# Performance work log

Measured on AMD Instinct MI355X. Metric: run time of the kernel, lower is better.

## Reference

```python
import jax, jax.numpy as jnp
from jax import lax
import numpy as np

DN = ('NCHW', 'OIHW', 'NCHW')
K = 3          # deformable kernel size
DG = 4         # deform groups
EXP = 4        # InvBottle expansion


def conv_offset(x, w1, w2, b2):
    """InvBottle with diff=True: depthwise-expanded 3x3 conv, diff correction, 1x1 conv."""
    B, C, H, W = x.shape
    _x = lax.conv_general_dilated(x, w1, (1, 1), ((1, 1), (1, 1)),
                                  dimension_numbers=DN, feature_group_count=C)  # [B,4C,H,W]
    # diff_conv: subtract grouped 1x1 conv with the kernel-summed weight
    wsum = w1.sum((2, 3)).reshape(1, EXP * C, 1, 1)          # [1,4C,1,1]
    xd = _x - jnp.repeat(x, EXP, axis=1) * wsum              # group g uses input channel g
    t = lax.conv_general_dilated(xd, w2, (1, 1), ((0, 0), (0, 0)), dimension_numbers=DN)
    return t + b2.reshape(1, -1, 1, 1)                       # [B,72,H,W]


def deform_depthwise(x, off, w, pad=1):
    """Depthwise DeformConv2d (groups=C, deform_groups=DG), stride=1, dilation=1."""
    B, C, H, W = x.shape
    Cg = C // DG
    off = off.reshape(B, DG, K * K, 2, H, W)                 # (dy, dx) interleaved per tap
    dy, dx = off[:, :, :, 0], off[:, :, :, 1]                # [B,DG,9,H,W]
    ky = (jnp.arange(K * K) // K).reshape(1, 1, K * K, 1, 1).astype(x.dtype)
    kx = (jnp.arange(K * K) % K).reshape(1, 1, K * K, 1, 1).astype(x.dtype)
    py = jnp.arange(H, dtype=x.dtype).reshape(1, 1, 1, H, 1) - pad + ky + dy
    px = jnp.arange(W, dtype=x.dtype).reshape(1, 1, 1, 1, W) - pad + kx + dx

    y0 = jnp.floor(py)
    x0 = jnp.floor(px)
    wy = py - y0
    wx = px - x0

    xg = x.reshape(B, DG, Cg, H * W)

    def gather(yy, xx):
        valid = ((yy >= 0) & (yy < H) & (xx >= 0) & (xx < W)).astype(x.dtype)
        yc = jnp.clip(yy, 0, H - 1).astype(jnp.int32)
        xc = jnp.clip(xx, 0, W - 1).astype(jnp.int32)
        idx = (yc * W + xc).reshape(B, DG, 1, K * K * H * W)
        v = jnp.take_along_axis(xg, jnp.broadcast_to(idx, (B, DG, Cg, K * K * H * W)), axis=3)
        return v.reshape(B, DG, Cg, K * K, H, W) * valid[:, :, None]

    val = (gather(y0, x0) * ((1 - wy) * (1 - wx))[:, :, None]
           + gather(y0, x0 + 1) * ((1 - wy) * wx)[:, :, None]
           + gather(y0 + 1, x0) * (wy * (1 - wx))[:, :, None]
           + gather(y0 + 1, x0 + 1) * (wy * wx)[:, :, None])   # [B,DG,Cg,9,H,W]

    val = val.reshape(B, C, K * K, H, W)
    return jnp.einsum('bckhw,ck->bchw', val, w.reshape(C, K * K))


def setup_inputs() -> dict:
    key = jax.random.key(0)
    ks = jax.random.split(key, 6)
    B, C, H, W = 2, 64, 192, 192
    x1 = jax.random.normal(ks[0], (B, C, H, W), jnp.float32)
    w_off1 = jax.random.normal(ks[1], (EXP * C, 1, K, K), jnp.float32) * 0.1
    w_off2 = jax.random.normal(ks[2], (DG * 2 * K * K, EXP * C, 1, 1), jnp.float32) * 0.1
    b_off2 = jax.random.normal(ks[3], (DG * 2 * K * K,), jnp.float32) * 0.1
    w_def = jax.random.normal(ks[4], (C, 1, K, K), jnp.float32) * 0.1
    w_out = jax.random.normal(ks[5], (C, C, 1, 1), jnp.float32) * 0.1
    return {'x1': x1, 'w_off1': w_off1, 'w_off2': w_off2, 'b_off2': b_off2,
            'w_def': w_def, 'w_out': w_out}


def reference(x1, w_off1, w_off2, b_off2, w_def, w_out):
    x2 = x1
    C = x1.shape[1]
    t = conv_offset(x1, w_off1, w_off2, b_off2)              # [B,72,H,W]
    y = deform_depthwise(x1, t, w_def)                       # DeformConv2d, groups=C
    # diff_conv against the deform conv's kernel-summed depthwise weight
    y = y - x2 * w_def.sum((1, 2, 3)).reshape(1, C, 1, 1)
    m = jnp.einsum('bchw,oc->bohw', y, w_out.reshape(w_out.shape[0], C))  # 1x1, no bias
    return (x1, m)
```

## Files before the change

### kernel.cpp

```cpp
#include <hip/hip_runtime.h>

#define BN   2
#define CN   64
#define HN   192
#define WN   192
#define HWN  36864
#define OCN  256
#define JCN  72
#define SN   32

#define DROWS 8
#define XH    17
#define XW    42
#define XRT   4
#define XCL   4

#define PGRPS 2304

typedef __attribute__((ext_vector_type(8))) short bf16x8;
typedef __attribute__((ext_vector_type(8))) unsigned short u16x8;
typedef __attribute__((ext_vector_type(4))) float f32x4;

__device__ __forceinline__ unsigned short f2bf(float f) {
    union { float f; unsigned u; } v; v.f = f;
    unsigned r = v.u + 0x7fffu + ((v.u >> 16) & 1u);
    return (unsigned short)(r >> 16);
}

__global__ __launch_bounds__(256) void k_prep(const float* __restrict__ w2,
                                              const float* __restrict__ w_out,
                                              const float* __restrict__ w1,
                                              unsigned short* __restrict__ w2mf,
                                              unsigned short* __restrict__ w_outmf,
                                              float* __restrict__ w1p) {
    int idx = blockIdx.x * 256 + threadIdx.x;
    if (idx < 20480) {
        int j  = idx & 7;
        int l  = (idx >> 3) & 63;
        int ts = idx >> 9;
        int tm = ts >> 3, s = ts & 7;
        int jrow = tm * 16 + (l & 15);
        int k    = s * 32 + (l >> 4) * 8 + j;
        float v = (jrow < JCN) ? w2[jrow * OCN + k] : 0.f;
        w2mf[idx] = f2bf(v);
    } else if (idx < 24576) {
        int r  = idx - 20480;
        int j  = r & 7;
        int l  = (r >> 3) & 63;
        int ts = r >> 9;
        int tm = ts >> 1, s = ts & 1;
        int m  = tm * 16 + (l & 15);
        int k  = s * 32 + (l >> 4) * 8 + j;
        w_outmf[r] = f2bf(w_out[m * CN + k]);
    } else if (idx < 26624) {
        int r = idx - 24576;
        int o = r >> 3, kk = r & 7;
        int k = kk < 4 ? kk : kk + 1;
        w1p[r] = w1[o * 9 + k];
    }
}

__global__ __launch_bounds__(256, 4) void k_offsets(const float* __restrict__ x,
                                                    const float* __restrict__ w1p,
                                                    const unsigned short* __restrict__ w2mf,
                                                    const float* __restrict__ b2,
                                                    float* __restrict__ t_out,
                                                    float* __restrict__ x_copy) {
    const int f  = blockIdx.x + 3 * blockIdx.y + 576 * blockIdx.z;
    const int nn = (f & 7) * 144 + (f >> 3);
    const int bx = nn % 3;
    const int by = (nn / 3) % 192;
    const int bz = nn / 576;

    const int tid  = threadIdx.x;
    const int wv   = tid >> 6;
    const int lane = tid & 63;
    const int q    = lane >> 4;
    const int n    = lane & 15;
    const int n0   = bx * 64 + wv * 16;
    const int y    = by;
    const int b    = bz;
    const int xcol = n0 + n;
    const float* xb = x + (size_t)b * CN * HWN;

    auto load_chunk = [&](int s, float (*ld)[9]) {
        #pragma unroll
        for (int cc = 0; cc < 2; ++cc) {
            int c = 8 * s + 2 * q + cc;
            const float* xp = xb + (size_t)c * HWN;
            #pragma unroll
            for (int k = 0; k < 9; ++k) {
                int ky = k / 3, kx = k - 3 * ky;
                int yy = y - 1 + ky, xx = xcol - 1 + kx;
                float v = 0.f;
                if ((unsigned)yy < (unsigned)HN && (unsigned)xx < (unsigned)WN)
                    v = xp[yy * WN + xx];
                ld[cc][k] = v;
            }
        }
    };

    f32x4 acc[5];
    #pragma unroll
    for (int t = 0; t < 5; ++t) acc[t] = (f32x4){0.f, 0.f, 0.f, 0.f};

    const bf16x8* ap = (const bf16x8*)w2mf + lane;

    float lbuf[2][2][9];
    load_chunk(0, lbuf[0]);
    #pragma unroll
    for (int s = 0; s < 8; ++s) {
        if (s < 7) load_chunk(s + 1, lbuf[(s + 1) & 1]);
        float (*ld)[9] = lbuf[s & 1];

        float dd[2][8];
        #pragma unroll
        for (int cc = 0; cc < 2; ++cc) {
            int c = 8 * s + 2 * q + cc;
            float ctr = ld[cc][4];
            x_copy[((size_t)b * CN + c) * HWN + y * WN + xcol] = ctr;
            #pragma unroll
            for (int kk = 0; kk < 8; ++kk) {
                int k = kk < 4 ? kk : kk + 1;
                dd[cc][kk] = ld[cc][k] - ctr;
            }
        }

        bf16x8 bfr;
        const float4* wp = (const float4*)(w1p + (size_t)(s * 32 + q * 8) * 8);
        #pragma unroll
        for (int j = 0; j < 8; ++j) {
            float4 wa = wp[2 * j];
            float4 wb = wp[2 * j + 1];
            const float* d = dd[j >> 2];
            float a = wa.x * d[0] + wa.y * d[1] + wa.z * d[2] + wa.w * d[3]
                    + wb.x * d[4] + wb.y * d[5] + wb.z * d[6] + wb.w * d[7];
            bfr[j] = (short)f2bf(a);
        }

        #pragma unroll
        for (int tm = 0; tm < 5; ++tm) {
            bf16x8 af = ap[(tm * 8 + s) * 64];
            acc[tm] = __builtin_amdgcn_mfma_f32_16x16x32_bf16(af, bfr, acc[tm], 0, 0, 0);
        }
    }

    float* tb = t_out + (size_t)b * JCN * HWN + y * WN + n0 + n;
    #pragma unroll
    for (int tm = 0; tm < 5; ++tm) {
        #pragma unroll
        for (int r = 0; r < 4; ++r) {
            int j = tm * 16 + q * 4 + r;
            if (j < JCN)
                tb[(size_t)j * HWN] = acc[tm][r] + b2[j];
        }
    }
}

__device__ __forceinline__ float dsample(const float* __restrict__ p, int yi, int xi) {
    if ((unsigned)yi < (unsigned)HN && (unsigned)xi < (unsigned)WN)
        return p[yi * WN + xi];
    return 0.f;
}

__global__ __launch_bounds__(256, 4) void k_deform(const float* __restrict__ x,
                                                   const float* __restrict__ t_in,
                                                   const float* __restrict__ wdef,
                                                   unsigned short* __restrict__ y_out) {
    __shared__ float xs[8 * XH * XW];
    __shared__ float wks[9 * 8];
    __shared__ float wsums[8];

    const int f    = blockIdx.x + 6 * blockIdx.y + 144 * blockIdx.z;
    const int slot = f >> 3;
    const int xcd  = f & 7;
    const int tile = slot >> 1;
    const int cm   = slot & 1;
    const int zz   = 2 * xcd + cm;
    const int bx   = tile % 6;
    const int byy  = tile / 6;

    const int x0   = bx * SN;
    const int yr0  = byy * DROWS;
    const int b    = zz >> 3;
    const int chunk = zz & 7;
    const int g    = chunk >> 1;
    const int tid  = threadIdx.x;
    const int r    = tid >> 5;
    const int px   = tid & 31;
    const int row_lo = yr0 - XRT;
    const int col_lo = x0 - XCL;
    const float* xb = x + (size_t)b * CN * HWN;

    float dyr[9], dxr[9];
    {
        const float* tbp = t_in + ((size_t)b * JCN + g * 18) * HWN
                         + (yr0 + r) * WN + x0 + px;
        #pragma unroll
        for (int k = 0; k < 9; ++k) {
            dyr[k] = tbp[(size_t)(2 * k) * HWN];
            dxr[k] = tbp[(size_t)(2 * k + 1) * HWN];
        }
    }

    for (int idx = tid; idx < 8 * XH * XW; idx += 256) {
        int cc  = idx / (XH * XW);
        int rem = idx - cc * (XH * XW);
        int rr  = rem / XW;
        int col = rem - rr * XW;
        int yy  = row_lo + rr;
        int xx  = col_lo + col;
        float v = 0.f;
        if ((unsigned)yy < (unsigned)HN && (unsigned)xx < (unsigned)WN)
            v = xb[(size_t)(chunk * 8 + cc) * HWN + yy * WN + xx];
        xs[idx] = v;
    }
    if (tid < 72) {
        int k = tid >> 3, cc = tid & 7;
        wks[tid] = wdef[(chunk * 8 + cc) * 9 + k];
    } else if (tid < 80) {
        int cc = tid - 72;
        float s = 0.f;
        #pragma unroll
        for (int k = 0; k < 9; ++k) s += wdef[(chunk * 8 + cc) * 9 + k];
        wsums[cc] = s;
    }
    __syncthreads();

    float acc[8];
    #pragma unroll
    for (int c = 0; c < 8; ++c)
        acc[c] = -xs[c * (XH * XW) + (XRT + r) * XW + XCL + px] * wsums[c];

    const float ry_basef = (float)(yr0 + r - 1);
    const float rx_basef = (float)(x0 + px - 1);

    #pragma unroll
    for (int k = 0; k < 9; ++k) {
        const int ky = k / 3, kx = k - 3 * ky;
        float py  = ry_basef + (float)ky + dyr[k];
        float pxf = rx_basef + (float)kx + dxr[k];
        float y0f = floorf(py), x0f = floorf(pxf);
        float wy = py - y0f, wx = pxf - x0f;
        int yi = (int)y0f, xi = (int)x0f;
        int ry = yi - row_lo, rx = xi - col_lo;
        float omwy = 1.f - wy, omwx = 1.f - wx;
        float w00 = omwy * omwx;
        float w01 = omwy * wx;
        float w10 = wy * omwx;
        float w11 = wy * wx;
        float4 wka = *(const float4*)&wks[k * 8];
        float4 wkb = *(const float4*)&wks[k * 8 + 4];
        float wkv[8] = {wka.x, wka.y, wka.z, wka.w, wkb.x, wkb.y, wkb.z, wkb.w};
        if ((unsigned)ry < (XH - 1) && (unsigned)rx < (XW - 1)) {
            const float* p0 = xs + ry * XW + rx;
            #pragma unroll
            for (int c = 0; c < 8; ++c) {
                const float* p = p0 + c * (XH * XW);
                float bil = p[0] * w00 + p[1] * w01 + p[XW] * w10 + p[XW + 1] * w11;
                acc[c] += wkv[c] * bil;
            }
        } else {
            #pragma unroll
            for (int c = 0; c < 8; ++c) {
                const float* xp = xb + (size_t)(chunk * 8 + c) * HWN;
                float v00 = dsample(xp, yi,     xi);
                float v01 = dsample(xp, yi,     xi + 1);
                float v10 = dsample(xp, yi + 1, xi);
                float v11 = dsample(xp, yi + 1, xi + 1);
                float bil = v00 * w00 + v01 * w01 + v10 * w10 + v11 * w11;
                acc[c] += wkv[c] * bil;
            }
        }
    }

    u16x8 pk;
    #pragma unroll
    for (int c = 0; c < 8; ++c) pk[c] = f2bf(acc[c]);
    const int P = (yr0 + r) * (WN / 16) + ((x0 + px) >> 4);
    unsigned short* yo = y_out
        + ((((size_t)b * PGRPS + P) * 2 + (chunk >> 2)) * 4 + (chunk & 3)) * 128
        + (px & 15) * 8;
    *(u16x8*)yo = pk;
}

__global__ __launch_bounds__(256, 8) void k_final(const unsigned short* __restrict__ y_bf,
                                                  const unsigned short* __restrict__ womf,
                                                  float* __restrict__ m_out) {
    const int tid  = threadIdx.x;
    const int wv   = tid >> 6;
    const int lane = tid & 63;
    const int q    = lane >> 4;
    const int n    = lane & 15;
    const int yr   = blockIdx.y;
    const int b    = blockIdx.z;
    const int P    = yr * (WN / 16) + blockIdx.x * 4 + wv;

    const unsigned short* yp = y_bf + ((size_t)b * PGRPS + P) * 1024;
    bf16x8 bfr0 = *(const bf16x8*)(yp + (0 * 64 + q * 16 + n) * 8);
    bf16x8 bfr1 = *(const bf16x8*)(yp + (1 * 64 + q * 16 + n) * 8);

    const bf16x8* ap = (const bf16x8*)womf + lane;
    f32x4 acc[4];
    #pragma unroll
    for (int tm = 0; tm < 4; ++tm) acc[tm] = (f32x4){0.f, 0.f, 0.f, 0.f};
    #pragma unroll
    for (int tm = 0; tm < 4; ++tm) {
        acc[tm] = __builtin_amdgcn_mfma_f32_16x16x32_bf16(ap[(tm * 2 + 0) * 64], bfr0, acc[tm], 0, 0, 0);
        acc[tm] = __builtin_amdgcn_mfma_f32_16x16x32_bf16(ap[(tm * 2 + 1) * 64], bfr1, acc[tm], 0, 0, 0);
    }

    float* mb = m_out + (size_t)b * CN * HWN + yr * WN + blockIdx.x * 64 + wv * 16 + n;
    #pragma unroll
    for (int tm = 0; tm < 4; ++tm) {
        #pragma unroll
        for (int r = 0; r < 4; ++r)
            mb[(size_t)(tm * 16 + q * 4 + r) * HWN] = acc[tm][r];
    }
}

extern "C" void kernel_launch(void* const* d_in, const int* in_sizes, int n_in,
                              void* d_out, int out_size, void* d_ws, size_t ws_size,
                              hipStream_t stream) {
    const float* x1    = (const float*)d_in[0];
    const float* w_off1 = (const float*)d_in[1];
    const float* w_off2 = (const float*)d_in[2];
    const float* b_off2 = (const float*)d_in[3];
    const float* w_def = (const float*)d_in[4];
    const float* w_out = (const float*)d_in[5];

    float* out = (float*)d_out;
    const size_t n_x = (size_t)BN * CN * HWN;
    float* out_x1 = out;
    float* out_m  = out + n_x;

    char* ws0 = (char*)d_ws;
    unsigned short* w2mf   = (unsigned short*)ws0;
    unsigned short* w_outmf = (unsigned short*)(ws0 + 40960);
    float* w1p    = (float*)(ws0 + 49152);
    float* t_ws   = (float*)(ws0 + 57344);
    unsigned short* y_bf = (unsigned short*)(ws0 + 57344 + 21233664);

    dim3 blk(256);

    k_prep<<<dim3(104), blk, 0, stream>>>(w_off2, w_out, w_off1, w2mf, w_outmf, w1p);
    k_offsets<<<dim3(WN / 64, HN, BN), blk, 0, stream>>>(x1, w1p, w2mf, b_off2,
                                                         t_ws, out_x1);
    k_deform<<<dim3(WN / SN, HN / DROWS, BN * 8), blk, 0, stream>>>(x1, t_ws, w_def, y_bf);
    k_final<<<dim3(WN / 64, HN, BN), blk, 0, stream>>>(y_bf, w_outmf, out_m);
}
```

Baseline: 170.1 us.

## Stage offset-conv input rows in shared memory instead of per-thread 3x3 global loads

k_offsets now cooperatively loads the three input rows (all 64 channels, 66 columns) into a shared-memory tile once per block, then reads the 3x3 neighbourhoods from LDS. This replaces the nine redundant global loads per thread per channel and the register double-buffering. The x_copy write is folded into the staging loop. It adds about 52KB of LDS per block and a barrier, lowers the occupancy hint from 4 to 3, and also changes XW in the deform kernel's tile padding.

Measured after the change: 193.6 us. 1.14x slower.

```diff
diff --git a/kernel.cpp b/kernel.cpp
--- a/kernel.cpp
+++ b/kernel.cpp
@@ -11,7 +11,7 @@
 
 #define DROWS 8
 #define XH    17
-#define XW    42
+#define XW    43
 #define XRT   4
 #define XCL   4
 
@@ -60,12 +60,14 @@
     }
 }
 
-__global__ __launch_bounds__(256, 4) void k_offsets(const float* __restrict__ x,
+__global__ __launch_bounds__(256, 3) void k_offsets(const float* __restrict__ x,
                                                     const float* __restrict__ w1p,
                                                     const unsigned short* __restrict__ w2mf,
                                                     const float* __restrict__ b2,
                                                     float* __restrict__ t_out,
                                                     float* __restrict__ x_copy) {
+    __shared__ float xsh[3][64][68];
+
     const int f  = blockIdx.x + 3 * blockIdx.y + 576 * blockIdx.z;
     const int nn = (f & 7) * 144 + (f >> 3);
     const int bx = nn % 3;
@@ -77,52 +79,53 @@
     const int lane = tid & 63;
     const int q    = lane >> 4;
     const int n    = lane & 15;
-    const int n0   = bx * 64 + wv * 16;
+    const int x0   = bx * 64;
     const int y    = by;
     const int b    = bz;
-    const int xcol = n0 + n;
     const float* xb = x + (size_t)b * CN * HWN;
 
-    auto load_chunk = [&](int s, float (*ld)[9]) {
+    for (int task = wv; task < 192; task += 4) {
+        const int rr = task >> 6;
+        const int c  = task & 63;
+        const int yy = y - 1 + rr;
+        const bool yok = (unsigned)yy < (unsigned)HN;
+        const float* xp = xb + (size_t)c * HWN + yy * WN;
+        const int xx = x0 - 1 + lane;
+        float v = (yok && (unsigned)xx < (unsigned)WN) ? xp[xx] : 0.f;
+        xsh[rr][c][lane] = v;
+        float v2 = 0.f;
+        if (lane < 2) {
+            const int xx2 = x0 + 63 + lane;
+            v2 = (yok && (unsigned)xx2 < (unsigned)WN) ? xp[xx2] : 0.f;
+            xsh[rr][c][64 + lane] = v2;
+        }
+        if (rr == 1) {
+            float* xcr = x_copy + ((size_t)b * CN + c) * HWN + (size_t)y * WN;
+            if (lane >= 1) xcr[xx] = v;
+            if (lane == 0) xcr[x0 + 63] = v2;
+        }
+    }
+    __syncthreads();
+
+    f32x4 acc[5];
+    #pragma unroll
+    for (int t = 0; t < 5; ++t) acc[t] = (f32x4){0.f, 0.f, 0.f, 0.f};
+
+    const bf16x8* ap = (const bf16x8*)w2mf + lane;
+    const int cb = wv * 16 + n;
+
+    #pragma unroll
+    for (int s = 0; s < 8; ++s) {
+        float dd[2][8];
         #pragma unroll
         for (int cc = 0; cc < 2; ++cc) {
-            int c = 8 * s + 2 * q + cc;
-            const float* xp = xb + (size_t)c * HWN;
-            #pragma unroll
-            for (int k = 0; k < 9; ++k) {
-                int ky = k / 3, kx = k - 3 * ky;
-                int yy = y - 1 + ky, xx = xcol - 1 + kx;
-                float v = 0.f;
-                if ((unsigned)yy < (unsigned)HN && (unsigned)xx < (unsigned)WN)
-                    v = xp[yy * WN + xx];
-                ld[cc][k] = v;
-            }
-        }
-    };
-
-    f32x4 acc[5];
-    #pragma unroll
-    for (int t = 0; t < 5; ++t) acc[t] = (f32x4){0.f, 0.f, 0.f, 0.f};
-
-    const bf16x8* ap = (const bf16x8*)w2mf + lane;
-
-    float lbuf[2][2][9];
-    load_chunk(0, lbuf[0]);
-    #pragma unroll
-    for (int s = 0; s < 8; ++s) {
-        if (s < 7) load_chunk(s + 1, lbuf[(s + 1) & 1]);
-        float (*ld)[9] = lbuf[s & 1];
-
-        float dd[2][8];
-        #pragma unroll
-        for (int cc = 0; cc < 2; ++cc) {
-            int c = 8 * s + 2 * q + cc;
-            float ctr = ld[cc][4];
-            x_copy[((size_t)b * CN + c) * HWN + y * WN + xcol] = ctr;
+            const int c = 8 * s + 2 * q + cc;
+            const float ctr = xsh[1][c][cb + 1];
             #pragma unroll
             for (int kk = 0; kk < 8; ++kk) {
-                int k = kk < 4 ? kk : kk + 1;
-                dd[cc][kk] = ld[cc][k] - ctr;
+                const int k  = kk < 4 ? kk : kk + 1;
+                const int ky = k / 3, kx = k - 3 * ky;
+                dd[cc][kk] = xsh[ky][c][cb + kx] - ctr;
             }
         }
 
@@ -145,7 +148,7 @@
         }
     }
 
-    float* tb = t_out + (size_t)b * JCN * HWN + y * WN + n0 + n;
+    float* tb = t_out + (size_t)b * JCN * HWN + y * WN + x0 + wv * 16 + n;
     #pragma unroll
     for (int tm = 0; tm < 5; ++tm) {
         #pragma unroll
```

## Split k_offsets channel reduction across two wave groups with LDS reduction

Applied to the files above, without the earlier changes.

The offset kernel now launches 512 threads per block. Two groups of four waves each handle half of the 64 input-channel chunks, so each wave runs 4 MFMA steps instead of 8. The second group writes its partial accumulators to shared memory, and the first group adds them before storing the offsets. This shortens the serial dependency chain per wave and raises parallelism, at the cost of about 21 KB of LDS, a block barrier, and lower block occupancy. The deform tile width XW is also padded from 42 to 43, likely to reduce LDS bank conflicts.

Result: faster. 165.5 us (-2.7%).

```diff
diff --git a/kernel.cpp b/kernel.cpp
--- a/kernel.cpp
+++ b/kernel.cpp
@@ -11,7 +11,7 @@
 
 #define DROWS 8
 #define XH    17
-#define XW    42
+#define XW    43
 #define XRT   4
 #define XCL   4
 
@@ -60,12 +60,14 @@
     }
 }
 
-__global__ __launch_bounds__(256, 4) void k_offsets(const float* __restrict__ x,
+__global__ __launch_bounds__(512, 4) void k_offsets(const float* __restrict__ x,
                                                     const float* __restrict__ w1p,
                                                     const unsigned short* __restrict__ w2mf,
                                                     const float* __restrict__ b2,
                                                     float* __restrict__ t_out,
                                                     float* __restrict__ x_copy) {
+    __shared__ float red[4 * 64 * 21];
+
     const int f  = blockIdx.x + 3 * blockIdx.y + 576 * blockIdx.z;
     const int nn = (f & 7) * 144 + (f >> 3);
     const int bx = nn % 3;
@@ -73,14 +75,16 @@
     const int bz = nn / 576;
 
     const int tid  = threadIdx.x;
-    const int wv   = tid >> 6;
+    const int wave = tid >> 6;
+    const int sgrp = wave >> 2;
+    const int wv   = wave & 3;
     const int lane = tid & 63;
     const int q    = lane >> 4;
     const int n    = lane & 15;
-    const int n0   = bx * 64 + wv * 16;
+    const int x0   = bx * 64;
     const int y    = by;
     const int b    = bz;
-    const int xcol = n0 + n;
+    const int xcol = x0 + wv * 16 + n;
     const float* xb = x + (size_t)b * CN * HWN;
 
     auto load_chunk = [&](int s, float (*ld)[9]) {
@@ -106,53 +110,70 @@
 
     const bf16x8* ap = (const bf16x8*)w2mf + lane;
 
-    float lbuf[2][2][9];
-    load_chunk(0, lbuf[0]);
-    #pragma unroll
-    for (int s = 0; s < 8; ++s) {
-        if (s < 7) load_chunk(s + 1, lbuf[(s + 1) & 1]);
-        float (*ld)[9] = lbuf[s & 1];
-
-        float dd[2][8];
-        #pragma unroll
-        for (int cc = 0; cc < 2; ++cc) {
-            int c = 8 * s + 2 * q + cc;
-            float ctr = ld[cc][4];
-            x_copy[((size_t)b * CN + c) * HWN + y * WN + xcol] = ctr;
-            #pragma unroll
-            for (int kk = 0; kk < 8; ++kk) {
-                int k = kk < 4 ? kk : kk + 1;
-                dd[cc][kk] = ld[cc][k] - ctr;
-            }
-        }
-
-        bf16x8 bfr;
-        const float4* wp = (const float4*)(w1p + (size_t)(s * 32 + q * 8) * 8);
-        #pragma unroll
-        for (int j = 0; j < 8; ++j) {
-            float4 wa = wp[2 * j];
-            float4 wb = wp[2 * j + 1];
-            const float* d = dd[j >> 2];
-            float a = wa.x * d[0] + wa.y * d[1] + wa.z * d[2] + wa.w * d[3]
-                    + wb.x * d[4] + wb.y * d[5] + wb.z * d[6] + wb.w * d[7];
-            bfr[j] = (short)f2bf(a);
-        }
-
+    #pragma unroll
+    for (int sgi = 0; sgi < 2; ++sgi) {
+        if (sgrp == sgi) {
+            float lbuf[2][2][9];
+            load_chunk(sgi * 4, lbuf[0]);
+            #pragma unroll
+            for (int ss = 0; ss < 4; ++ss) {
+                const int s = sgi * 4 + ss;
+                if (ss < 3) load_chunk(s + 1, lbuf[(ss + 1) & 1]);
+                float (*ld)[9] = lbuf[ss & 1];
+
+                float dd[2][8];
+                #pragma unroll
+                for (int cc = 0; cc < 2; ++cc) {
+                    int c = 8 * s + 2 * q + cc;
+                    float ctr = ld[cc][4];
+                    x_copy[((size_t)b * CN + c) * HWN + y * WN + xcol] = ctr;
+                    #pragma unroll
+                    for (int kk = 0; kk < 8; ++kk) {
+                        int k = kk < 4 ? kk : kk + 1;
+                        dd[cc][kk] = ld[cc][k] - ctr;
+                    }
+                }
+
+                bf16x8 bfr;
+                const float4* wp = (const float4*)(w1p + (size_t)(s * 32 + q * 8) * 8);
+                #pragma unroll
+                for (int j = 0; j < 8; ++j) {
+                    float4 wa = wp[2 * j];
+                    float4 wb = wp[2 * j + 1];
+                    const float* d = dd[j >> 2];
+                    float a = wa.x * d[0] + wa.y * d[1] + wa.z * d[2] + wa.w * d[3]
+                            + wb.x * d[4] + wb.y * d[5] + wb.z * d[6] + wb.w * d[7];
+                    bfr[j] = (short)f2bf(a);
+                }
+
+                #pragma unroll
+                for (int tm = 0; tm < 5; ++tm) {
+                    bf16x8 af = ap[(tm * 8 + s) * 64];
+                    acc[tm] = __builtin_amdgcn_mfma_f32_16x16x32_bf16(af, bfr, acc[tm], 0, 0, 0);
+                }
+            }
+        }
+    }
+
+    float* rp = &red[(wv * 64 + lane) * 21];
+    if (sgrp == 1) {
+        #pragma unroll
+        for (int tm = 0; tm < 5; ++tm)
+            #pragma unroll
+            for (int r = 0; r < 4; ++r)
+                rp[tm * 4 + r] = acc[tm][r];
+    }
+    __syncthreads();
+    if (sgrp == 0) {
+        float* tb = t_out + (size_t)b * JCN * HWN + y * WN + x0 + wv * 16 + n;
         #pragma unroll
         for (int tm = 0; tm < 5; ++tm) {
-            bf16x8 af = ap[(tm * 8 + s) * 64];
-            acc[tm] = __builtin_amdgcn_mfma_f32_16x16x32_bf16(af, bfr, acc[tm], 0, 0, 0);
-        }
-    }
-
-    float* tb = t_out + (size_t)b * JCN * HWN + y * WN + n0 + n;
-    #pragma unroll
-    for (int tm = 0; tm < 5; ++tm) {
-        #pragma unroll
-        for (int r = 0; r < 4; ++r) {
-            int j = tm * 16 + q * 4 + r;
-            if (j < JCN)
-                tb[(size_t)j * HWN] = acc[tm][r] + b2[j];
+            #pragma unroll
+            for (int r = 0; r < 4; ++r) {
+                int j = tm * 16 + q * 4 + r;
+                if (j < JCN)
+                    tb[(size_t)j * HWN] = acc[tm][r] + rp[tm * 4 + r] + b2[j];
+            }
         }
     }
 }
@@ -341,11 +362,9 @@
     float* t_ws   = (float*)(ws0 + 57344);
     unsigned short* y_bf = (unsigned short*)(ws0 + 57344 + 21233664);
 
-    dim3 blk(256);
-
-    k_prep<<<dim3(104), blk, 0, stream>>>(w_off2, w_out, w_off1, w2mf, w_outmf, w1p);
-    k_offsets<<<dim3(WN / 64, HN, BN), blk, 0, stream>>>(x1, w1p, w2mf, b_off2,
-                                                         t_ws, out_x1);
-    k_deform<<<dim3(WN / SN, HN / DROWS, BN * 8), blk, 0, stream>>>(x1, t_ws, w_def, y_bf);
-    k_final<<<dim3(WN / 64, HN, BN), blk, 0, stream>>>(y_bf, w_outmf, out_m);
-}
+    k_prep<<<dim3(104), dim3(256), 0, stream>>>(w_off2, w_out, w_off1, w2mf, w_outmf, w1p);
+    k_offsets<<<dim3(WN / 64, HN, BN), dim3(512), 0, stream>>>(x1, w1p, w2mf, b_off2,
+                                                               t_ws, out_x1);
+    k_deform<<<dim3(WN / SN, HN / DROWS, BN * 8), dim3(256), 0, stream>>>(x1, t_ws, w_def, y_bf);
+    k_final<<<dim3(WN / 64, HN, BN), dim3(256), 0, stream>>>(y_bf, w_outmf, out_m);
+}
```
